# Optimization experiments

Hardware: AMD Instinct MI355X
Metric: run time of the kernel (lower is better)

Reference implementation:

```python
import jax, jax.numpy as jnp
import numpy as np

B, CIN, BINS, FRAMES = 8, 2, 1024, 512
NQ = 4
C = 2 * NQ          # number of quantizer channels
E = 1024            # codebook size
BETA = 0.25         # commitment cost


def conv2d(x, w, b, pad):
    y = jax.lax.conv_general_dilated(
        x, w, window_strides=(1, 1),
        padding=((pad[0], pad[0]), (pad[1], pad[1])),
        dimension_numbers=("NCHW", "OIHW", "NCHW"))
    return y + b[None, :, None, None]


def setup_inputs() -> dict:
    key = jax.random.key(0)
    ks = jax.random.split(key, 6)
    return {
        "x": jax.random.normal(ks[0], (B, CIN, BINS, FRAMES), jnp.float32),
        "conv1_w": jax.random.normal(ks[1], (C, CIN, 9, 1), jnp.float32) * 0.1,
        "conv1_b": jnp.zeros((C,), jnp.float32),
        "conv2_w": jax.random.normal(ks[2], (C, C, 9, 1), jnp.float32) * 0.05,
        "conv2_b": jnp.zeros((C,), jnp.float32),
        "skip_w": jax.random.normal(ks[3], (C, CIN, 1, 1), jnp.float32) * 0.1,
        "skip_b": jnp.zeros((C,), jnp.float32),
        "codebooks": jax.random.normal(ks[4], (C, E, BINS), jnp.float32),
    }


def reference(x, conv1_w, conv1_b, conv2_w, conv2_b, skip_w, skip_b, codebooks):
    # ResBlock projection: 2 -> 2*num_quantizers channels, (9,1) convs along bins
    h = conv2d(x, conv1_w, conv1_b, (4, 0))
    h = jax.nn.leaky_relu(h, 0.2)
    h = conv2d(h, conv2_w, conv2_b, (4, 0))
    h = h + conv2d(x, skip_w, skip_b, (0, 0))          # [B, C, BINS, F]

    # Batched VQ across all C quantizers at once.
    # Per-frame vectors: [C, N, BINS] with N = B*FRAMES
    v = jnp.transpose(h, (1, 0, 3, 2)).reshape(C, B * FRAMES, BINS)
    x2 = jnp.sum(v * v, axis=-1, keepdims=True)                     # [C,N,1]
    e2 = jnp.sum(codebooks * codebooks, axis=-1)[:, None, :]        # [C,1,E]
    d = x2 + e2 - 2.0 * jnp.einsum("cnb,ceb->cne", v, codebooks)    # [C,N,E]
    idx = jnp.argmin(d, axis=-1)                                    # [C,N]
    q = jax.vmap(lambda cb, i: cb[i])(codebooks, idx)               # [C,N,BINS]

    # VQ-VAE loss (codebook + commitment), summed over the 2Q quantizers
    sg = jax.lax.stop_gradient
    cb_loss = jnp.mean((q - sg(v)) ** 2, axis=(1, 2))
    cm_loss = jnp.mean((sg(q) - v) ** 2, axis=(1, 2))
    loss = jnp.sum(cb_loss + BETA * cm_loss)

    # straight-through estimator
    q_st = v + sg(q - v)                                            # [C,N,BINS]
    q_st = q_st.reshape(C, B, FRAMES, BINS).transpose(1, 0, 3, 2)   # [B,C,BINS,F]
    # torch loop prepends each new q: final channel order is reversed
    embedded = q_st[:, ::-1]
    return embedded, loss
```

## Files before the change

kernel.cpp:

```cpp
#include <hip/hip_runtime.h>

namespace {

constexpr int kB = 8, kCin = 2, kBins = 1024, kFrames = 512;
constexpr int kC = 8, kE = 1024, kN = kB * kFrames;

typedef _Float16 f16x8 __attribute__((ext_vector_type(8)));
typedef float f32x4 __attribute__((ext_vector_type(4)));

union HPack4 { _Float16 h[4]; uint2 u; };

__device__ inline void splitf(float v, _Float16& h, _Float16& l) {
    float a = (fabsf(v) >= 6.103515625e-05f) ? v : 0.f;
    _Float16 hh = (_Float16)a;
    h = hh;
    l = (_Float16)((v - (float)hh) * 4096.0f);
}

constexpr int BT = 32, FT = 32, XB = BT + 16, HB = BT + 8;

__global__ __launch_bounds__(256) void conv_fused_v2(
    const float* __restrict__ x,
    const float* __restrict__ w1, const float* __restrict__ b1,
    const float* __restrict__ w2, const float* __restrict__ b2,
    const float* __restrict__ wsk, const float* __restrict__ bsk,
    _Float16* __restrict__ V1, float* __restrict__ partials)
{
    __shared__ float xt[kCin][XB][33];
    __shared__ float h1t[kC][HB][33];
    __shared__ float vbuf[BT][33];
    __shared__ float w1s[kC * kCin * 9];
    __shared__ float w2s[kC * kC][12];
    __shared__ float wsks[kC * kCin];
    __shared__ float b1s[kC], b2s[kC], bsks[kC];
    __shared__ float reds[256];

    const int t = threadIdx.x;
    const int bt = blockIdx.x, ft = blockIdx.y, bb = blockIdx.z;
    const int bs = bt * BT, f0 = ft * FT;
    _Float16* V2 = V1 + (size_t)33554432;

    for (int i = t; i < kC * kCin * 9; i += 256) w1s[i] = w1[i];
    for (int i = t; i < 768; i += 256) {
        int cc = i / 12, k = i % 12;
        w2s[cc][k] = (k < 9) ? w2[cc * 9 + k] : 0.f;
    }
    if (t < kC * kCin) wsks[t] = wsk[t];
    if (t < kC) { b1s[t] = b1[t]; b2s[t] = b2[t]; bsks[t] = bsk[t]; }

    for (int i = t; i < kCin * XB * FT; i += 256) {
        int fi = i % FT, xb = (i / FT) % XB, ci = i / (FT * XB);
        int gb = bs - 8 + xb;
        float v = 0.f;
        if (gb >= 0 && gb < kBins)
            v = x[((bb * kCin + ci) * kBins + gb) * kFrames + f0 + fi];
        xt[ci][xb][fi] = v;
    }
    __syncthreads();

    const int fi = t & 31;
    const int r = t >> 5;

    for (int q = 0; q < 5; q++) {
        float a8[8];
        #pragma unroll
        for (int jj = 0; jj < 8; jj++) a8[jj] = b1s[r];
        #pragma unroll
        for (int ci = 0; ci < kCin; ci++) {
            float w[16];
            #pragma unroll
            for (int k = 0; k < 16; k++) w[k] = xt[ci][q * 8 + k][fi];
            const float* wp = &w1s[(r * kCin + ci) * 9];
            #pragma unroll
            for (int jj = 0; jj < 8; jj++)
                #pragma unroll
                for (int k = 0; k < 9; k++)
                    a8[jj] += w[jj + k] * wp[k];
        }
        #pragma unroll
        for (int jj = 0; jj < 8; jj++) {
            int hb = q * 8 + jj;
            int gb = bs - 4 + hb;
            float v = (gb >= 0 && gb < kBins) ? (a8[jj] > 0.f ? a8[jj] : 0.2f * a8[jj]) : 0.f;
            h1t[r][hb][fi] = v;
        }
    }
    __syncthreads();

    float acc[8][4];
    #pragma unroll
    for (int c = 0; c < 8; c++)
        #pragma unroll
        for (int j = 0; j < 4; j++) acc[c][j] = b2s[c] + bsks[c];

    for (int ci = 0; ci < 8; ci++) {
        float w[12];
        #pragma unroll
        for (int k = 0; k < 12; k++) w[k] = h1t[ci][r * 4 + k][fi];
        #pragma unroll
        for (int c = 0; c < 8; c++) {
            const float4* wp4 = (const float4*)&w2s[c * 8 + ci][0];
            float4 wA = wp4[0], wB = wp4[1], wC = wp4[2];
            float wk[9] = {wA.x, wA.y, wA.z, wA.w, wB.x, wB.y, wB.z, wB.w, wC.x};
            #pragma unroll
            for (int j = 0; j < 4; j++) {
                float s = 0.f;
                #pragma unroll
                for (int k = 0; k < 9; k++) s += w[j + k] * wk[k];
                acc[c][j] += s;
            }
        }
    }
    #pragma unroll
    for (int j = 0; j < 4; j++) {
        float x0 = xt[0][r * 4 + j + 8][fi];
        float x1 = xt[1][r * 4 + j + 8][fi];
        #pragma unroll
        for (int c = 0; c < 8; c++)
            acc[c][j] += x0 * wsks[c * 2] + x1 * wsks[c * 2 + 1];
    }

    float sq = 0.f;
    #pragma unroll
    for (int c = 0; c < 8; c++)
        #pragma unroll
        for (int j = 0; j < 4; j++) sq += acc[c][j] * acc[c][j];

    const int rr = t >> 3, q = t & 7;
    for (int c = 0; c < 8; c++) {
        __syncthreads();
        #pragma unroll
        for (int j = 0; j < 4; j++) vbuf[r * 4 + j][fi] = acc[c][j];
        __syncthreads();
        HPack4 ph, pl;
        #pragma unroll
        for (int j = 0; j < 4; j++) {
            float v = vbuf[q * 4 + j][rr];
            splitf(v, ph.h[j], pl.h[j]);
        }
        const int n = bb * kFrames + f0 + rr;
        const size_t off = ((size_t)(c * kN + n)) * kBins + bs + q * 4;
        *(uint2*)&V1[off] = ph.u;
        *(uint2*)&V2[off] = pl.u;
    }

    reds[t] = sq;
    __syncthreads();
    for (int off = 128; off > 0; off >>= 1) {
        if (t < off) reds[t] += reds[t + off];
        __syncthreads();
    }
    if (t == 0) {
        int blin = (bb * gridDim.y + blockIdx.y) * gridDim.x + blockIdx.x;
        partials[blin] = reds[0];
    }
}

__global__ __launch_bounds__(256) void cbsplit_e2(
    const float* __restrict__ cb, _Float16* __restrict__ B1,
    float* __restrict__ e2)
{
    const int gw = (blockIdx.x * 256 + threadIdx.x) >> 6;
    const int lane = threadIdx.x & 63;
    _Float16* B2 = B1 + (size_t)8388608;
    const float* row = cb + (size_t)gw * kBins;
    float s = 0.f;
    #pragma unroll
    for (int j = 0; j < 4; j++) {
        float4 v = *(const float4*)&row[lane * 4 + j * 256];
        s += v.x * v.x + v.y * v.y + v.z * v.z + v.w * v.w;
        HPack4 ph, pl;
        splitf(v.x, ph.h[0], pl.h[0]);
        splitf(v.y, ph.h[1], pl.h[1]);
        splitf(v.z, ph.h[2], pl.h[2]);
        splitf(v.w, ph.h[3], pl.h[3]);
        size_t off = (size_t)gw * kBins + lane * 4 + j * 256;
        *(uint2*)&B1[off] = ph.u;
        *(uint2*)&B2[off] = pl.u;
    }
    #pragma unroll
    for (int off = 32; off > 0; off >>= 1) s += __shfl_down(s, off);
    if (lane == 0) e2[gw] = s;
}

__global__ __launch_bounds__(256, 1) void dist_mfma(
    const _Float16* __restrict__ V1, const _Float16* __restrict__ B1p,
    const float* __restrict__ e2, unsigned long long* __restrict__ pk)
{
    __shared__ char smem[4 * 32768 + 2048];

    const int t = threadIdx.x;
    const int bidx = blockIdx.x;
    const int ch = bidx & 7;
    const int eh = (bidx >> 3) & 1;
    const int n0 = (bidx >> 4) * 128;
    const int w = t >> 6, lane = t & 63;
    const int l15 = lane & 15, kc4 = lane >> 4;
    const int wm = w >> 1, we = w & 1;

    float* lds_e2 = (float*)(smem + 131072);
    {
        const float* e2c = e2 + ch * kE + eh * 512;
        lds_e2[t] = e2c[t];
        lds_e2[t + 256] = e2c[t + 256];
    }

    const _Float16* srcA[4];
    const _Float16* srcB[4];
    int dstoff[4];
    #pragma unroll
    for (int i = 0; i < 4; i++) {
        int ci = w * 256 + i * 64 + lane;
        int row = ci >> 3, slot = ci & 7;
        int g = slot ^ (row & 7);
        int p = g >> 2, kc = g & 3;
        srcA[i] = V1 + (size_t)p * 33554432 + ((size_t)(ch * kN + n0 + row)) * kBins + kc * 8;
        srcB[i] = B1p + (size_t)p * 8388608 + ((size_t)(ch * kE + row)) * kBins + kc * 8;
        dstoff[i] = (w * 256 + i * 64) * 16;
    }

    const int rowA = wm * 64 + l15;
    const int rowB = we * 64 + l15;
    const int baseA1 = rowA * 128 + ((kc4) ^ (rowA & 7)) * 16;
    const int baseA2 = rowA * 128 + ((4 + kc4) ^ (rowA & 7)) * 16;
    const int baseB1 = 16384 + rowB * 128 + ((kc4) ^ (rowB & 7)) * 16;
    const int baseB2 = 16384 + rowB * 128 + ((4 + kc4) ^ (rowB & 7)) * 16;

    float rm[16];
    int ri[16];
    #pragma unroll
    for (int s = 0; s < 16; s++) { rm[s] = 3.4e38f; ri[s] = 0; }

    typedef const __attribute__((address_space(1))) void gsrc_t;
    typedef __attribute__((address_space(3))) void gdst_t;

    auto issue = [&](int jj) {
        const int k0 = (jj & 31) * 32;
        const size_t etoff = (size_t)(eh * 4 + (jj >> 5)) * 128 * kBins + k0;
        char* nb = smem + (jj & 3) * 32768;
        #pragma unroll
        for (int i = 0; i < 4; i++)
            __builtin_amdgcn_global_load_lds((gsrc_t*)(srcA[i] + k0), (gdst_t*)(nb + dstoff[i]), 16, 0, 0);
        #pragma unroll
        for (int i = 0; i < 4; i++)
            __builtin_amdgcn_global_load_lds((gsrc_t*)(srcB[i] + etoff), (gdst_t*)(nb + 16384 + dstoff[i]), 16, 0, 0);
    };

    f32x4 hi[4][4], lo[4][4];
    #pragma unroll
    for (int mi = 0; mi < 4; mi++)
        #pragma unroll
        for (int ei = 0; ei < 4; ei++) {
            hi[mi][ei] = (f32x4){0.f, 0.f, 0.f, 0.f};
            lo[mi][ei] = (f32x4){0.f, 0.f, 0.f, 0.f};
        }

    __syncthreads();

    issue(0); issue(1); issue(2);

    #pragma unroll 1
    for (int et = 0; et < 4; et++) {
        #pragma unroll 1
        for (int ks = 0; ks < 32; ks++) {
            const int j = et * 32 + ks;
            asm volatile("s_waitcnt vmcnt(16)\n\ts_barrier" ::: "memory");
            if (j < 125) issue(j + 3);

            const char* buf = smem + (j & 3) * 32768;
            f16x8 a1[4], a2[4], b1f[4], b2f[4];
            #pragma unroll
            for (int mi = 0; mi < 4; mi++) {
                a1[mi] = *(const f16x8*)(buf + baseA1 + mi * 2048);
                a2[mi] = *(const f16x8*)(buf + baseA2 + mi * 2048);
            }
            #pragma unroll
            for (int ei = 0; ei < 4; ei++) {
                b1f[ei] = *(const f16x8*)(buf + baseB1 + ei * 2048);
                b2f[ei] = *(const f16x8*)(buf + baseB2 + ei * 2048);
            }
            #pragma unroll
            for (int mi = 0; mi < 4; mi++)
                #pragma unroll
                for (int ei = 0; ei < 4; ei++) {
                    hi[mi][ei] = __builtin_amdgcn_mfma_f32_16x16x32_f16(a1[mi], b1f[ei], hi[mi][ei], 0, 0, 0);
                    lo[mi][ei] = __builtin_amdgcn_mfma_f32_16x16x32_f16(a1[mi], b2f[ei], lo[mi][ei], 0, 0, 0);
                    lo[mi][ei] = __builtin_amdgcn_mfma_f32_16x16x32_f16(a2[mi], b1f[ei], lo[mi][ei], 0, 0, 0);
                }
        }

        #pragma unroll
        for (int ei = 0; ei < 4; ei++) {
            const int eloc = et * 128 + we * 64 + ei * 16 + l15;
            const float ev = lds_e2[eloc];
            const int eix = eh * 512 + eloc;
            #pragma unroll
            for (int mi = 0; mi < 4; mi++) {
                f32x4 dot4 = hi[mi][ei] + lo[mi][ei] * (1.0f / 4096.0f);
                #pragma unroll
                for (int rr = 0; rr < 4; rr++) {
                    float d = ev - 2.0f * dot4[rr];
                    int s = mi * 4 + rr;
                    if (d < rm[s]) { rm[s] = d; ri[s] = eix; }
                }
                hi[mi][ei] = (f32x4){0.f, 0.f, 0.f, 0.f};
                lo[mi][ei] = (f32x4){0.f, 0.f, 0.f, 0.f};
            }
        }
    }

    #pragma unroll
    for (int m = 1; m < 16; m <<= 1) {
        #pragma unroll
        for (int s = 0; s < 16; s++) {
            float ov = __shfl_xor(rm[s], m);
            int oi = __shfl_xor(ri[s], m);
            if (ov < rm[s] || (ov == rm[s] && oi < ri[s])) { rm[s] = ov; ri[s] = oi; }
        }
    }

    float* mv = (float*)smem;
    int* miv = (int*)(smem + 1024);
    if (l15 == 0) {
        #pragma unroll
        for (int s = 0; s < 16; s++) {
            int mi = s >> 2, rr = s & 3;
            int rloc = wm * 64 + mi * 16 + (lane >> 4) * 4 + rr;
            mv[rloc * 2 + we] = rm[s];
            miv[rloc * 2 + we] = ri[s];
        }
    }
    __syncthreads();
    if (t < 128) {
        float v0 = mv[t * 2], v1 = mv[t * 2 + 1];
        int i0 = miv[t * 2], i1 = miv[t * 2 + 1];
        bool take1 = (v1 < v0) || (v1 == v0 && i1 < i0);
        float bv = take1 ? v1 : v0;
        int bi = take1 ? i1 : i0;
        unsigned int u = __float_as_uint(bv);
        unsigned int su = (u & 0x80000000u) ? ~u : (u ^ 0x80000000u);
        unsigned long long packed = ((unsigned long long)su << 32) | (unsigned int)bi;
        atomicMin(&pk[ch * kN + n0 + t], packed);
    }
}

__global__ __launch_bounds__(256) void gather_pk(
    const float* __restrict__ cb, const unsigned long long* __restrict__ pk,
    float* __restrict__ out)
{
    const int t = threadIdx.x;
    const int lane = t & 63, q = t >> 6;
    const int bt = blockIdx.x & 63;
    const int ftile = blockIdx.x >> 6;
    const int co = blockIdx.y, bb = blockIdx.z;
    const int cp = (kC - 1) - co;
    const int f = ftile * 64 + lane;
    const int n = bb * kFrames + f;
    const int e = (int)(unsigned int)(pk[cp * kN + n] & 0xFFFFFFFFull);
    const int bin0 = bt * 16 + q * 4;
    const float4 v4 = *(const float4*)&cb[((size_t)cp * kE + e) * kBins + bin0];
    const size_t base = ((size_t)(bb * kC + co) * kBins + bin0) * kFrames + f;
    out[base] = v4.x;
    out[base + kFrames] = v4.y;
    out[base + 2 * (size_t)kFrames] = v4.z;
    out[base + 3 * (size_t)kFrames] = v4.w;
}

__global__ __launch_bounds__(256) void finalize_loss_pk(
    const unsigned long long* __restrict__ pk, const float* __restrict__ partials,
    int npart, float* __restrict__ loss)
{
    __shared__ float reds[256];
    const int t = threadIdx.x;
    float s = 0.f;
    for (int i = t; i < kC * kN; i += 256) {
        unsigned int su = (unsigned int)(pk[i] >> 32);
        unsigned int u = (su & 0x80000000u) ? (su ^ 0x80000000u) : ~su;
        s += __uint_as_float(u);
    }
    for (int i = t; i < npart; i += 256) s += partials[i];
    reds[t] = s;
    __syncthreads();
    for (int off = 128; off > 0; off >>= 1) {
        if (t < off) reds[t] += reds[t + off];
        __syncthreads();
    }
    if (t == 0) loss[0] = 1.25f * reds[0] / (float)(kN * kBins);
}

}

extern "C" void kernel_launch(void* const* d_in, const int* in_sizes, int n_in,
                              void* d_out, int out_size, void* d_ws, size_t ws_size,
                              hipStream_t stream)
{
    const float* x   = (const float*)d_in[0];
    const float* w1  = (const float*)d_in[1];
    const float* b1  = (const float*)d_in[2];
    const float* w2  = (const float*)d_in[3];
    const float* b2  = (const float*)d_in[4];
    const float* wsk = (const float*)d_in[5];
    const float* bsk = (const float*)d_in[6];
    const float* cb  = (const float*)d_in[7];
    float* out = (float*)d_out;
    char* ws = (char*)d_ws;

    _Float16* B1 = (_Float16*)ws;
    float* e2                  = (float*)(ws + 33554432);
    unsigned long long* pk     = (unsigned long long*)(ws + 33554432 + 32768);
    float* partials            = (float*)(ws + 33554432 + 32768 + 262144);
    _Float16* V1 = (_Float16*)d_out;

    hipMemsetAsync(pk, 0xFF, (size_t)kC * kN * 8, stream);
    conv_fused_v2<<<dim3(kBins / BT, kFrames / FT, kB), 256, 0, stream>>>(
        x, w1, b1, w2, b2, wsk, bsk, V1, partials);
    cbsplit_e2<<<(kC * kE) / 4, 256, 0, stream>>>(cb, B1, e2);
    dist_mfma<<<dim3(512), 256, 0, stream>>>(V1, B1, e2, pk);
    gather_pk<<<dim3(512, kC, kB), 256, 0, stream>>>(cb, pk, out);
    finalize_loss_pk<<<1, 256, 0, stream>>>(pk, partials, 4096,
                                            out + (size_t)kC * kBins * kN);
}
```

Before: 446.8 us.

## Load MFMA operands directly from global memory and remap gather block order

The distance kernel drops its 4-stage LDS pipeline fed by global_load_lds and now reads f16 fragments straight from global memory into registers. LDS use shrinks to a small reduction buffer, and launch bounds go to 2 blocks per CU to allow more occupancy. The gather kernel is relaunched on a flat 1D grid with the channel index in the low bits, so consecutive blocks touch different codebooks. This gives up LDS reuse across waves, and the many redundant uncoalesced 16-byte global loads could hurt bandwidth.

```diff
diff --git a/kernel.cpp b/kernel.cpp
--- a/kernel.cpp
+++ b/kernel.cpp
@@ -183,11 +183,12 @@
     if (lane == 0) e2[gw] = s;
 }
 
-__global__ __launch_bounds__(256, 1) void dist_mfma(
+__global__ __launch_bounds__(256, 2) void dist_mfma(
     const _Float16* __restrict__ V1, const _Float16* __restrict__ B1p,
     const float* __restrict__ e2, unsigned long long* __restrict__ pk)
 {
-    __shared__ char smem[4 * 32768 + 2048];
+    __shared__ float mv[256];
+    __shared__ int miv[256];
 
     const int t = threadIdx.x;
     const int bidx = blockIdx.x;
@@ -198,86 +199,43 @@
     const int l15 = lane & 15, kc4 = lane >> 4;
     const int wm = w >> 1, we = w & 1;
 
-    float* lds_e2 = (float*)(smem + 131072);
-    {
-        const float* e2c = e2 + ch * kE + eh * 512;
-        lds_e2[t] = e2c[t];
-        lds_e2[t + 256] = e2c[t + 256];
-    }
-
-    const _Float16* srcA[4];
-    const _Float16* srcB[4];
-    int dstoff[4];
-    #pragma unroll
-    for (int i = 0; i < 4; i++) {
-        int ci = w * 256 + i * 64 + lane;
-        int row = ci >> 3, slot = ci & 7;
-        int g = slot ^ (row & 7);
-        int p = g >> 2, kc = g & 3;
-        srcA[i] = V1 + (size_t)p * 33554432 + ((size_t)(ch * kN + n0 + row)) * kBins + kc * 8;
-        srcB[i] = B1p + (size_t)p * 8388608 + ((size_t)(ch * kE + row)) * kBins + kc * 8;
-        dstoff[i] = (w * 256 + i * 64) * 16;
-    }
-
-    const int rowA = wm * 64 + l15;
-    const int rowB = we * 64 + l15;
-    const int baseA1 = rowA * 128 + ((kc4) ^ (rowA & 7)) * 16;
-    const int baseA2 = rowA * 128 + ((4 + kc4) ^ (rowA & 7)) * 16;
-    const int baseB1 = 16384 + rowB * 128 + ((kc4) ^ (rowB & 7)) * 16;
-    const int baseB2 = 16384 + rowB * 128 + ((4 + kc4) ^ (rowB & 7)) * 16;
+    const _Float16* pa1 = V1 + ((size_t)(ch * kN + n0 + wm * 64 + l15)) * kBins + kc4 * 8;
+    const _Float16* pa2 = pa1 + (size_t)33554432;
+    const _Float16* pb1base = B1p + ((size_t)(ch * kE + eh * 512 + we * 64 + l15)) * kBins + kc4 * 8;
+    const float* e2c = e2 + ch * kE;
 
     float rm[16];
     int ri[16];
     #pragma unroll
     for (int s = 0; s < 16; s++) { rm[s] = 3.4e38f; ri[s] = 0; }
 
-    typedef const __attribute__((address_space(1))) void gsrc_t;
-    typedef __attribute__((address_space(3))) void gdst_t;
-
-    auto issue = [&](int jj) {
-        const int k0 = (jj & 31) * 32;
-        const size_t etoff = (size_t)(eh * 4 + (jj >> 5)) * 128 * kBins + k0;
-        char* nb = smem + (jj & 3) * 32768;
-        #pragma unroll
-        for (int i = 0; i < 4; i++)
-            __builtin_amdgcn_global_load_lds((gsrc_t*)(srcA[i] + k0), (gdst_t*)(nb + dstoff[i]), 16, 0, 0);
-        #pragma unroll
-        for (int i = 0; i < 4; i++)
-            __builtin_amdgcn_global_load_lds((gsrc_t*)(srcB[i] + etoff), (gdst_t*)(nb + 16384 + dstoff[i]), 16, 0, 0);
-    };
-
-    f32x4 hi[4][4], lo[4][4];
-    #pragma unroll
-    for (int mi = 0; mi < 4; mi++)
-        #pragma unroll
-        for (int ei = 0; ei < 4; ei++) {
-            hi[mi][ei] = (f32x4){0.f, 0.f, 0.f, 0.f};
-            lo[mi][ei] = (f32x4){0.f, 0.f, 0.f, 0.f};
-        }
-
-    __syncthreads();
-
-    issue(0); issue(1); issue(2);
-
     #pragma unroll 1
     for (int et = 0; et < 4; et++) {
+        const _Float16* pb1 = pb1base + (size_t)et * 128 * kBins;
+        const _Float16* pb2 = pb1 + (size_t)8388608;
+
+        f32x4 hi[4][4], lo[4][4];
+        #pragma unroll
+        for (int mi = 0; mi < 4; mi++)
+            #pragma unroll
+            for (int ei = 0; ei < 4; ei++) {
+                hi[mi][ei] = (f32x4){0.f, 0.f, 0.f, 0.f};
+                lo[mi][ei] = (f32x4){0.f, 0.f, 0.f, 0.f};
+            }
+
         #pragma unroll 1
         for (int ks = 0; ks < 32; ks++) {
-            const int j = et * 32 + ks;
-            asm volatile("s_waitcnt vmcnt(16)\n\ts_barrier" ::: "memory");
-            if (j < 125) issue(j + 3);
-
-            const char* buf = smem + (j & 3) * 32768;
+            const int ko = ks * 32;
             f16x8 a1[4], a2[4], b1f[4], b2f[4];
             #pragma unroll
             for (int mi = 0; mi < 4; mi++) {
-                a1[mi] = *(const f16x8*)(buf + baseA1 + mi * 2048);
-                a2[mi] = *(const f16x8*)(buf + baseA2 + mi * 2048);
+                a1[mi] = *(const f16x8*)(pa1 + (size_t)mi * 16 * kBins + ko);
+                a2[mi] = *(const f16x8*)(pa2 + (size_t)mi * 16 * kBins + ko);
             }
             #pragma unroll
             for (int ei = 0; ei < 4; ei++) {
-                b1f[ei] = *(const f16x8*)(buf + baseB1 + ei * 2048);
-                b2f[ei] = *(const f16x8*)(buf + baseB2 + ei * 2048);
+                b1f[ei] = *(const f16x8*)(pb1 + (size_t)ei * 16 * kBins + ko);
+                b2f[ei] = *(const f16x8*)(pb2 + (size_t)ei * 16 * kBins + ko);
             }
             #pragma unroll
             for (int mi = 0; mi < 4; mi++)
@@ -291,9 +249,8 @@
 
         #pragma unroll
         for (int ei = 0; ei < 4; ei++) {
-            const int eloc = et * 128 + we * 64 + ei * 16 + l15;
-            const float ev = lds_e2[eloc];
-            const int eix = eh * 512 + eloc;
+            const int eix = eh * 512 + et * 128 + we * 64 + ei * 16 + l15;
+            const float ev = e2c[eix];
             #pragma unroll
             for (int mi = 0; mi < 4; mi++) {
                 f32x4 dot4 = hi[mi][ei] + lo[mi][ei] * (1.0f / 4096.0f);
@@ -303,8 +260,6 @@
                     int s = mi * 4 + rr;
                     if (d < rm[s]) { rm[s] = d; ri[s] = eix; }
                 }
-                hi[mi][ei] = (f32x4){0.f, 0.f, 0.f, 0.f};
-                lo[mi][ei] = (f32x4){0.f, 0.f, 0.f, 0.f};
             }
         }
     }
@@ -319,8 +274,6 @@
         }
     }
 
-    float* mv = (float*)smem;
-    int* miv = (int*)(smem + 1024);
     if (l15 == 0) {
         #pragma unroll
         for (int s = 0; s < 16; s++) {
@@ -350,10 +303,12 @@
 {
     const int t = threadIdx.x;
     const int lane = t & 63, q = t >> 6;
-    const int bt = blockIdx.x & 63;
-    const int ftile = blockIdx.x >> 6;
-    const int co = blockIdx.y, bb = blockIdx.z;
-    const int cp = (kC - 1) - co;
+    const int b = blockIdx.x;
+    const int cp = b & 7;
+    const int bt = (b >> 3) & 63;
+    const int ftile = (b >> 9) & 7;
+    const int bb = b >> 12;
+    const int co = (kC - 1) - cp;
     const int f = ftile * 64 + lane;
     const int n = bb * kFrames + f;
     const int e = (int)(unsigned int)(pk[cp * kN + n] & 0xFFFFFFFFull);
@@ -416,7 +371,7 @@
         x, w1, b1, w2, b2, wsk, bsk, V1, partials);
     cbsplit_e2<<<(kC * kE) / 4, 256, 0, stream>>>(cb, B1, e2);
     dist_mfma<<<dim3(512), 256, 0, stream>>>(V1, B1, e2, pk);
-    gather_pk<<<dim3(512, kC, kB), 256, 0, stream>>>(cb, pk, out);
+    gather_pk<<<dim3(32768), 256, 0, stream>>>(cb, pk, out);
     finalize_loss_pk<<<1, 256, 0, stream>>>(pk, partials, 4096,
                                             out + (size_t)kC * kBins * kN);
 }
```

New measurement: 693.5 us. 55.2% more time.
